# Kernel tuning notes

Measured on AMD Instinct MI355X. Metric: run time of the kernel, lower is better.

Reference implementation:

```python
import jax, jax.numpy as jnp
import numpy as np

TMP1 = 0.01
TMP2 = 0.1
TMP3 = 0.1
NEG_MARGIN = 0.1  # referenced in source forward but never set in __init__; fixed here
CLAMP_MAX = 88.0


def setup_inputs() -> dict:
    key = jax.random.key(0)
    scores = jax.random.normal(key, (512, 8192), dtype=jnp.float32)
    k_vals = jnp.array([1, 5, 10], dtype=jnp.int32)
    return {"scores": scores, "k_vals": k_vals, "pos_num": 16}


def reference(scores, k_vals, pos_num):
    # scores: [B, N]; first `pos_num` columns are positives (gt == 1), rest negatives.
    P = pos_num
    K = k_vals.shape[0]
    pos = scores[:, :P]          # [B, P]
    neg = scores[:, P:]          # [B, N-P]

    # pairwise diffs: pos rows and neg rows of the per-sample [N, P] diff matrix
    pos_diff = pos[:, :, None] - pos[:, None, :]                    # [B, P, P]
    neg_diff = neg[:, :, None] - pos[:, None, :] + NEG_MARGIN       # [B, N-P, P]

    # negative rows: soft step via temperature-scaled softplus, two-sided
    neg_term = jnp.where(
        neg_diff >= 0,
        jnp.logaddexp(0.0, neg_diff / TMP2) + 0.1,
        jnp.logaddexp(0.0, neg_diff / TMP1),
    )                                                               # [B, N-P, P]

    # positive rows: hard indicator (detached in source), zero the diagonal
    eye = jnp.eye(P, dtype=scores.dtype)
    pos_term = (pos_diff >= 0).astype(scores.dtype) * (1.0 - eye)   # [B, P, P]

    # soft rank of each positive: 1 + sum over all rows
    rank = 1.0 + pos_term.sum(axis=1) + neg_term.sum(axis=1)        # [B, P]

    # soft recall@k penalty per positive and cutoff
    z = (rank[:, :, None] - k_vals[None, None, :].astype(scores.dtype)) / TMP3
    recall = jnp.logaddexp(0.0, jnp.minimum(z, CLAMP_MAX))          # [B, P, K]

    per_sample = recall.sum(axis=(1, 2)) / (P * K)                  # [B]
    return per_sample.mean()
```

## Files before the change

### kernel.cpp

```cpp
#include <hip/hip_runtime.h>
#include <hip/hip_bf16.h>


#define ROWS 512
#define COLS 8192
#define POSN 16
#define NK 3
#define NCHUNK 4
#define NEG_PER_CHUNK 2044
#define NF4 511

__global__ __launch_bounds__(256)
void negsum_kernel(const float* __restrict__ scores, float* __restrict__ ws)
{
    const int b     = blockIdx.x;
    const int row   = b >> 2;
    const int chunk = b & 3;
    const int wave  = threadIdx.x >> 6;
    const int lane  = threadIdx.x & 63;
    const float* rowp = scores + (size_t)row * COLS;

    const float C10 = 14.4269504089f;
    const float A0  = 1.44269504089f;
    const float LN2 = 0.69314718056f;

    float p10[4];
#pragma unroll
    for (int jj = 0; jj < 4; ++jj)
        p10[jj] = rowp[wave * 4 + jj] * C10;

    float acc[4] = {0.0f, 0.0f, 0.0f, 0.0f};

    const float4* negs =
        reinterpret_cast<const float4*>(rowp + POSN + chunk * NEG_PER_CHUNK);

#pragma unroll 2
    for (int it = 0; it < 8; ++it) {
        const int f = it * 64 + lane;
        if (f < NF4) {
            const float4 v = negs[f];
            float a10[4];
            a10[0] = __fmaf_rn(v.x, C10, A0);
            a10[1] = __fmaf_rn(v.y, C10, A0);
            a10[2] = __fmaf_rn(v.z, C10, A0);
            a10[3] = __fmaf_rn(v.w, C10, A0);
#pragma unroll
            for (int e = 0; e < 4; ++e) {
#pragma unroll
                for (int jj = 0; jj < 4; ++jj) {
                    const float t10  = a10[e] - p10[jj];
                    const float t100 = 10.0f * t10;
                    const float arg  = fminf(-t10, t100);
                    const float ex   = exp2f(arg);
                    const float l    = __log2f(1.0f + ex);
                    float lin        = __fmaf_rn(t10, LN2, 0.1f);
                    lin              = (t10 >= 0.0f) ? lin : 0.0f;
                    acc[jj] += lin;
                    acc[jj]  = __fmaf_rn(l, LN2, acc[jj]);
                }
            }
        }
    }

#pragma unroll
    for (int jj = 0; jj < 4; ++jj) {
        float s = acc[jj];
#pragma unroll
        for (int off = 32; off > 0; off >>= 1)
            s += __shfl_xor(s, off);
        acc[jj] = s;
    }

    if (lane == 0) {
        float* o = ws + ((size_t)(chunk * ROWS + row)) * POSN + wave * 4;
        o[0] = acc[0]; o[1] = acc[1]; o[2] = acc[2]; o[3] = acc[3];
    }
}

__global__ __launch_bounds__(256)
void finalize_kernel(const float* __restrict__ scores,
                     const float* __restrict__ ws,
                     const int* __restrict__ k_vals,
                     float* __restrict__ out)
{
    const int gid = blockIdx.x * 256 + threadIdx.x;
    const int row = gid >> 4;
    const int j   = gid & 15;
    const float* rowp = scores + (size_t)row * COLS;

    float negsum = 0.0f;
#pragma unroll
    for (int c = 0; c < NCHUNK; ++c)
        negsum += ws[((size_t)(c * ROWS + row)) * POSN + j];

    const float pj = rowp[j];
    float cnt = -1.0f;
#pragma unroll
    for (int i = 0; i < POSN; ++i)
        cnt += (rowp[i] >= pj) ? 1.0f : 0.0f;

    const float rank = 1.0f + cnt + negsum;

    float rsum = 0.0f;
#pragma unroll
    for (int k = 0; k < NK; ++k) {
        float z = (rank - (float)k_vals[k]) * 10.0f;
        z = fminf(z, 88.0f);
        const float e = exp2f(-1.44269504089f * fabsf(z));
        rsum += fmaxf(z, 0.0f) + 0.69314718056f * __log2f(1.0f + e);
    }

    const int wave = threadIdx.x >> 6;
    const int lane = threadIdx.x & 63;
#pragma unroll
    for (int off = 32; off > 0; off >>= 1)
        rsum += __shfl_xor(rsum, off);

    __shared__ float sp[4];
    if (lane == 0) sp[wave] = rsum;
    __syncthreads();
    if (threadIdx.x == 0) {
        const float s = sp[0] + sp[1] + sp[2] + sp[3];
        atomicAdd(out, s * (1.0f / ((float)POSN * (float)NK * (float)ROWS)));
    }
}

extern "C" void kernel_launch(void* const* d_in, const int* in_sizes, int n_in,
                              void* d_out, int out_size, void* d_ws, size_t ws_size,
                              hipStream_t stream) {
    const float* scores = (const float*)d_in[0];
    const int*   k_vals = (const int*)d_in[1];
    float* out = (float*)d_out;
    float* ws  = (float*)d_ws;

    hipMemsetAsync(out, 0, sizeof(float), stream);
    negsum_kernel<<<ROWS * NCHUNK, 256, 0, stream>>>(scores, ws);
    finalize_kernel<<<(ROWS * POSN) / 256, 256, 0, stream>>>(scores, ws, k_vals, out);
}
```

Measured before the change: 97.01 us.

## Replace per-element log with running product of softplus terms

The negsum kernel now accumulates the product of (1+exp2(arg)) across the 32 elements each lane handles and takes a single log at the end, instead of one log per element. The linear part is split into a max(t,0) sum plus a count of non-negative terms times 0.1. All loads are issued upfront into registers, with a clamped index and the out-of-range lane masked by a very negative sentinel. Raw amdgcn exp2/log builtins replace the library calls and an occupancy hint is added. The running product risks overflow or precision loss across 32 factors.

```diff
diff --git a/kernel.cpp b/kernel.cpp
--- a/kernel.cpp
+++ b/kernel.cpp
@@ -1,5 +1,4 @@
 #include <hip/hip_runtime.h>
-#include <hip/hip_bf16.h>
 
 
 #define ROWS 512
@@ -7,10 +6,11 @@
 #define POSN 16
 #define NK 3
 #define NCHUNK 4
-#define NEG_PER_CHUNK 2044
-#define NF4 511
+#define CHUNK_F4 511
 
-__global__ __launch_bounds__(256)
+typedef float f32x4 __attribute__((ext_vector_type(4)));
+
+__global__ __launch_bounds__(256, 6)
 void negsum_kernel(const float* __restrict__ scores, float* __restrict__ ws)
 {
     const int b     = blockIdx.x;
@@ -22,58 +22,62 @@
 
     const float C10 = 14.4269504089f;
     const float A0  = 1.44269504089f;
-    const float LN2 = 0.69314718056f;
+    const float LN2 = 0.69314718055994531f;
 
     float p10[4];
 #pragma unroll
     for (int jj = 0; jj < 4; ++jj)
         p10[jj] = rowp[wave * 4 + jj] * C10;
 
-    float acc[4] = {0.0f, 0.0f, 0.0f, 0.0f};
+    const f32x4* negs =
+        reinterpret_cast<const f32x4*>(rowp + POSN) + (size_t)chunk * CHUNK_F4;
 
-    const float4* negs =
-        reinterpret_cast<const float4*>(rowp + POSN + chunk * NEG_PER_CHUNK);
+    f32x4 v[8];
+#pragma unroll
+    for (int it = 0; it < 8; ++it) {
+        int f = it * 64 + lane;
+        if (f > CHUNK_F4 - 1) f = CHUNK_F4 - 1;
+        v[it] = negs[f];
+    }
+    if (lane == 63) {
+        v[7].x = -1.0e30f; v[7].y = -1.0e30f; v[7].z = -1.0e30f; v[7].w = -1.0e30f;
+    }
 
-#pragma unroll 2
+    float prod[4] = {1.f, 1.f, 1.f, 1.f};
+    float accM[4] = {0.f, 0.f, 0.f, 0.f};
+    int   ncnt[4] = {0, 0, 0, 0};
+
+#pragma unroll
     for (int it = 0; it < 8; ++it) {
-        const int f = it * 64 + lane;
-        if (f < NF4) {
-            const float4 v = negs[f];
-            float a10[4];
-            a10[0] = __fmaf_rn(v.x, C10, A0);
-            a10[1] = __fmaf_rn(v.y, C10, A0);
-            a10[2] = __fmaf_rn(v.z, C10, A0);
-            a10[3] = __fmaf_rn(v.w, C10, A0);
+        float a10[4];
+        a10[0] = __fmaf_rn(v[it].x, C10, A0);
+        a10[1] = __fmaf_rn(v[it].y, C10, A0);
+        a10[2] = __fmaf_rn(v[it].z, C10, A0);
+        a10[3] = __fmaf_rn(v[it].w, C10, A0);
 #pragma unroll
-            for (int e = 0; e < 4; ++e) {
+        for (int e = 0; e < 4; ++e) {
 #pragma unroll
-                for (int jj = 0; jj < 4; ++jj) {
-                    const float t10  = a10[e] - p10[jj];
-                    const float t100 = 10.0f * t10;
-                    const float arg  = fminf(-t10, t100);
-                    const float ex   = exp2f(arg);
-                    const float l    = __log2f(1.0f + ex);
-                    float lin        = __fmaf_rn(t10, LN2, 0.1f);
-                    lin              = (t10 >= 0.0f) ? lin : 0.0f;
-                    acc[jj] += lin;
-                    acc[jj]  = __fmaf_rn(l, LN2, acc[jj]);
-                }
+            for (int jj = 0; jj < 4; ++jj) {
+                const float t   = a10[e] - p10[jj];
+                const float arg = fminf(-t, 10.0f * t);
+                const float u   = __builtin_amdgcn_exp2f(arg);
+                prod[jj] = __fmaf_rn(prod[jj], u, prod[jj]);
+                accM[jj] += fmaxf(t, 0.0f);
+                ncnt[jj] += (int)(__float_as_uint(t) >> 31);
             }
         }
     }
 
 #pragma unroll
     for (int jj = 0; jj < 4; ++jj) {
-        float s = acc[jj];
+        const float nge = 32.0f - (float)ncnt[jj];
+        float s = __fmaf_rn(accM[jj] + __builtin_amdgcn_logf(prod[jj]),
+                            LN2, 0.1f * nge);
 #pragma unroll
         for (int off = 32; off > 0; off >>= 1)
             s += __shfl_xor(s, off);
-        acc[jj] = s;
-    }
-
-    if (lane == 0) {
-        float* o = ws + ((size_t)(chunk * ROWS + row)) * POSN + wave * 4;
-        o[0] = acc[0]; o[1] = acc[1]; o[2] = acc[2]; o[3] = acc[3];
+        if (lane == 0)
+            ws[((size_t)(chunk * ROWS + row)) * POSN + wave * 4 + jj] = s;
     }
 }
 
@@ -106,8 +110,9 @@
     for (int k = 0; k < NK; ++k) {
         float z = (rank - (float)k_vals[k]) * 10.0f;
         z = fminf(z, 88.0f);
-        const float e = exp2f(-1.44269504089f * fabsf(z));
-        rsum += fmaxf(z, 0.0f) + 0.69314718056f * __log2f(1.0f + e);
+        const float e2 = __builtin_amdgcn_exp2f(-1.44269504089f * fabsf(z));
+        rsum += fmaxf(z, 0.0f)
+              + 0.69314718056f * __builtin_amdgcn_logf(1.0f + e2);
     }
 
     const int wave = threadIdx.x >> 6;
```

After: 83.72 us. 13.7% less time.
